# Optimization experiments

Hardware: AMD Instinct MI355X
Metric: run time of the kernel (lower is better)

The kernel has to match this reference:

```python
import jax, jax.numpy as jnp
import numpy as np

B, S, D, H = 2, 2048, 1024, 16
DK = D // H

def setup_inputs() -> dict:
    key = jax.random.key(0)
    ks = jax.random.split(key, 10)
    s = 1.0 / np.sqrt(D)
    x = jax.random.normal(ks[0], (B, S, D), dtype=jnp.float32)
    # causal mask [B,1,S,S]: 1 = keep, 0 = masked
    mask = jnp.broadcast_to(jnp.tril(jnp.ones((S, S), dtype=jnp.int32))[None, None], (B, 1, S, S))
    wq = jax.random.uniform(ks[1], (D, D), jnp.float32, -s, s)
    bq = jax.random.uniform(ks[2], (D,), jnp.float32, -s, s)
    wk = jax.random.uniform(ks[3], (D, D), jnp.float32, -s, s)
    bk = jax.random.uniform(ks[4], (D,), jnp.float32, -s, s)
    wv = jax.random.uniform(ks[5], (D, D), jnp.float32, -s, s)
    bv = jax.random.uniform(ks[6], (D,), jnp.float32, -s, s)
    wo = jax.random.uniform(ks[7], (D, D), jnp.float32, -s, s)
    bo = jax.random.uniform(ks[8], (D,), jnp.float32, -s, s)
    return {"x": x, "mask": mask, "wq": wq, "bq": bq, "wk": wk, "bk": bk,
            "wv": wv, "bv": bv, "wo": wo, "bo": bo}

def reference(x, mask, wq, bq, wk, bk, wv, bv, wo, bo):
    # projections; torch Linear: y = x @ W^T + b
    def proj(w, b):
        return (jnp.einsum('bsd,ed->bse', x, w) + b).reshape(B, S, H, DK).transpose(0, 2, 1, 3)
    q = proj(wq, bq)  # [B,H,S,DK]
    k = proj(wk, bk)
    v = proj(wv, bv)
    scores = jnp.einsum('bhsd,bhtd->bhst', q, k) / np.sqrt(DK)  # [B,H,S,S]
    scores = jnp.where(mask == 0, jnp.float32(-1e9), scores)
    attn = jax.nn.softmax(scores, axis=-1)
    # dropout in eval mode -> identity
    out = jnp.einsum('bhst,bhtd->bhsd', attn, v)  # [B,H,S,DK]
    out = out.transpose(0, 2, 1, 3).reshape(B, S, D)
    return jnp.einsum('bsd,ed->bse', out, wo) + bo
```

## Files before the change

kernel.cpp:

```cpp
#include <hip/hip_runtime.h>
#include <hip/hip_bf16.h>

#define BB 2
#define SS 2048
#define DD 1024
#define HH 16
#define DK 64
#define MM (BB*SS)

typedef __attribute__((ext_vector_type(8))) short bf16x8;
typedef __attribute__((ext_vector_type(4))) float f32x4;

__device__ inline ushort f2bf(float f) {
  __hip_bfloat16 h = __float2bfloat16(f);
  return *reinterpret_cast<ushort*>(&h);
}

__device__ __forceinline__ float exp2_hw(float x) {
  float r; asm("v_exp_f32 %0, %1" : "=v"(r) : "v"(x)); return r;
}

__device__ __forceinline__ void gl_lds16(const ushort* g, ushort* l) {
  __builtin_amdgcn_global_load_lds((const __attribute__((address_space(1))) void*)g,
                                   (__attribute__((address_space(3))) void*)l, 16, 0, 0);
}

__global__ void cvt_f32_bf16(const float* __restrict__ src, ushort* __restrict__ dst, int n4) {
  int i = blockIdx.x * blockDim.x + threadIdx.x;
  int stride = gridDim.x * blockDim.x;
  for (int idx = i; idx < n4; idx += stride) {
    float4 v = reinterpret_cast<const float4*>(src)[idx];
    ushort4 o;
    o.x = f2bf(v.x); o.y = f2bf(v.y); o.z = f2bf(v.z); o.w = f2bf(v.w);
    reinterpret_cast<ushort4*>(dst)[idx] = o;
  }
}

__global__ void cvt3_f32_bf16(const float* __restrict__ s0, const float* __restrict__ s1,
                              const float* __restrict__ s2, ushort* __restrict__ dst) {
  const int n4seg = DD * DD / 4;
  int i = blockIdx.x * blockDim.x + threadIdx.x;
  int stride = gridDim.x * blockDim.x;
  for (int idx = i; idx < 3 * n4seg; idx += stride) {
    int seg = idx / n4seg;
    int off = idx - seg * n4seg;
    const float* s = (seg == 0) ? s0 : (seg == 1) ? s1 : s2;
    float4 v = reinterpret_cast<const float4*>(s)[off];
    ushort4 o;
    o.x = f2bf(v.x); o.y = f2bf(v.y); o.z = f2bf(v.z); o.w = f2bf(v.w);
    reinterpret_cast<ushort4*>(dst)[idx] = o;
  }
}

__global__ void cvt5_f32_bf16(const float* __restrict__ x,
                              const float* __restrict__ s0, const float* __restrict__ s1,
                              const float* __restrict__ s2, const float* __restrict__ s3,
                              ushort* __restrict__ dx, ushort* __restrict__ dw) {
  const int n4x = MM * DD / 4;
  const int n4seg = DD * DD / 4;
  const int total = n4x + 4 * n4seg;
  int i = blockIdx.x * blockDim.x + threadIdx.x;
  int stride = gridDim.x * blockDim.x;
  for (int idx = i; idx < total; idx += stride) {
    float4 v; ushort4* outp;
    if (idx < n4x) {
      v = reinterpret_cast<const float4*>(x)[idx];
      outp = &reinterpret_cast<ushort4*>(dx)[idx];
    } else {
      int widx = idx - n4x;
      int seg = widx / n4seg;
      int off = widx - seg * n4seg;
      const float* s = (seg == 0) ? s0 : (seg == 1) ? s1 : (seg == 2) ? s2 : s3;
      v = reinterpret_cast<const float4*>(s)[off];
      outp = &reinterpret_cast<ushort4*>(dw)[widx];
    }
    ushort4 o;
    o.x = f2bf(v.x); o.y = f2bf(v.y); o.z = f2bf(v.z); o.w = f2bf(v.w);
    *outp = o;
  }
}

__global__ __launch_bounds__(256, 3) void gemm_qkv(const ushort* __restrict__ A,
                                                   const ushort* __restrict__ Wqkv,
                                                   const float* __restrict__ bq,
                                                   const float* __restrict__ bk,
                                                   const float* __restrict__ bv,
                                                   ushort* __restrict__ Qo,
                                                   ushort* __restrict__ Ko,
                                                   ushort* __restrict__ Vo,
                                                   float qscale) {
  constexpr int K = 1024;
  __shared__ __align__(16) ushort lS[2][128 * 64];
  ushort* lA = lS[0];
  ushort* lB = lS[1];
  const int t = threadIdx.x;
  const int w = t >> 6, lane = t & 63;
  const int flat = blockIdx.x + 24 * blockIdx.y;
  const int xcd = flat & 7, idx = flat >> 3;
  const int m0 = ((xcd << 2) + (idx & 3)) * 128;
  const int n0 = (idx >> 2) * 128;
  const int wm = (w >> 1) * 64, wn = (w & 1) * 64;
  const int c = lane & 15, g = lane >> 4;

  f32x4 acc[4][4];
  #pragma unroll
  for (int i = 0; i < 4; i++)
    #pragma unroll
    for (int j = 0; j < 4; j++) acc[i][j] = f32x4{0.f, 0.f, 0.f, 0.f};

  auto stage = [&](int ks) {
    const int k0 = ks * 64;
    #pragma unroll
    for (int i = 0; i < 4; i++) {
      int ch = w * 256 + i * 64 + lane;
      int row = ch >> 3;
      int cs = (ch & 7) ^ (row & 7);
      gl_lds16(&A[(size_t)(m0 + row) * K + k0 + cs * 8], &lA[(w * 256 + i * 64) * 8]);
      gl_lds16(&Wqkv[(size_t)(n0 + row) * K + k0 + cs * 8], &lB[(w * 256 + i * 64) * 8]);
    }
  };

  for (int ks = 0; ks < 16; ks++) {
    stage(ks);
    __syncthreads();
    #pragma unroll
    for (int kk2 = 0; kk2 < 2; kk2++) {
      bf16x8 af[4], bfr[4];
      #pragma unroll
      for (int mi = 0; mi < 4; mi++) {
        int row = wm + mi * 16 + c;
        af[mi] = *reinterpret_cast<const bf16x8*>(&lA[row * 64 + (((kk2 * 4 + g) ^ (c & 7)) * 8)]);
      }
      #pragma unroll
      for (int ni = 0; ni < 4; ni++) {
        int row = wn + ni * 16 + c;
        bfr[ni] = *reinterpret_cast<const bf16x8*>(&lB[row * 64 + (((kk2 * 4 + g) ^ (c & 7)) * 8)]);
      }
      #pragma unroll
      for (int mi = 0; mi < 4; mi++)
        #pragma unroll
        for (int ni = 0; ni < 4; ni++)
          acc[mi][ni] = __builtin_amdgcn_mfma_f32_16x16x32_bf16(af[mi], bfr[ni], acc[mi][ni], 0, 0, 0);
    }
    __syncthreads();
  }

  const int seg = n0 >> 10;
  const float* bp = (seg == 0) ? bq : (seg == 1) ? bk : bv;
  const float sc = (seg == 0) ? qscale : 1.0f;
  ushort* lC = &lS[0][0];

  if (seg < 2) {
    #pragma unroll
    for (int mi = 0; mi < 4; mi++) {
      #pragma unroll
      for (int ni = 0; ni < 4; ni++) {
        int col = wn + ni * 16 + c;
        float bvv = bp[(n0 + col) & 1023];
        #pragma unroll
        for (int j = 0; j < 4; j++) {
          int row = wm + mi * 16 + g * 4 + j;
          lC[row * 128 + col] = f2bf((acc[mi][ni][j] + bvv) * sc);
        }
      }
    }
    __syncthreads();
    ushort* op = (seg == 0) ? Qo : Ko;
    const int b = m0 >> 11, s0r = m0 & 2047;
    #pragma unroll
    for (int i = 0; i < 8; i++) {
      int id = i * 256 + t;
      int row = id >> 4, colblk = id & 15;
      ushort4 v0 = *reinterpret_cast<const ushort4*>(&lC[row * 128 + colblk * 8]);
      ushort4 v1 = *reinterpret_cast<const ushort4*>(&lC[row * 128 + colblk * 8 + 4]);
      int colq = (n0 + colblk * 8) & 1023;
      int h = colq >> 6, dkb = colq & 63;
      ushort* dst = &op[(((size_t)(b * HH + h) * SS + s0r + row) << 6) + dkb];
      reinterpret_cast<ushort4*>(dst)[0] = v0;
      reinterpret_cast<ushort4*>(dst)[1] = v1;
    }
  } else {
    #pragma unroll
    for (int mi = 0; mi < 4; mi++) {
      #pragma unroll
      for (int ni = 0; ni < 4; ni++) {
        int col = wn + ni * 16 + c;
        float bvv = bp[(n0 + col) & 1023];
        int rowbase = wm + mi * 16 + g * 4;
        ushort4 pk;
        pk.x = f2bf(acc[mi][ni][0] + bvv);
        pk.y = f2bf(acc[mi][ni][1] + bvv);
        pk.z = f2bf(acc[mi][ni][2] + bvv);
        pk.w = f2bf(acc[mi][ni][3] + bvv);
        *reinterpret_cast<ushort4*>(&lC[col * 128 + rowbase]) = pk;
      }
    }
    __syncthreads();
    const int b = m0 >> 11, s0r = m0 & 2047;
    #pragma unroll
    for (int i = 0; i < 8; i++) {
      int id = i * 256 + t;
      int col = id >> 4, rowblk = id & 15;
      ushort4 v0 = *reinterpret_cast<const ushort4*>(&lC[col * 128 + rowblk * 8]);
      ushort4 v1 = *reinterpret_cast<const ushort4*>(&lC[col * 128 + rowblk * 8 + 4]);
      int colq = (n0 + col) & 1023;
      int h = colq >> 6, dk = colq & 63;
      ushort* dst = &Vo[(((size_t)(b * HH + h) * DK + dk) << 11) + s0r + rowblk * 8];
      reinterpret_cast<ushort4*>(dst)[0] = v0;
      reinterpret_cast<ushort4*>(dst)[1] = v1;
    }
  }
}

__global__ __launch_bounds__(256, 4) void gemm_out(const ushort* __restrict__ A,
                                                   const ushort* __restrict__ W,
                                                   const float* __restrict__ bias,
                                                   float* __restrict__ out) {
  constexpr int K = 1024;
  __shared__ __align__(16) ushort lA[64 * 64];
  __shared__ __align__(16) ushort lB[64 * 64];
  const int t = threadIdx.x;
  const int w = t >> 6, lane = t & 63;
  const int flat = blockIdx.x + 16 * blockIdx.y;
  const int xcd = flat & 7, idx = flat >> 3;
  const int m0 = ((xcd << 3) + (idx & 7)) * 64;
  const int n0 = (idx >> 3) * 64;
  const int wm = (w >> 1) * 32, wn = (w & 1) * 32;
  const int c = lane & 15, g = lane >> 4;

  f32x4 acc[2][2];
  #pragma unroll
  for (int i = 0; i < 2; i++)
    #pragma unroll
    for (int j = 0; j < 2; j++) acc[i][j] = f32x4{0.f, 0.f, 0.f, 0.f};

  auto stage = [&](int ks) {
    const int k0 = ks * 64;
    #pragma unroll
    for (int i = 0; i < 2; i++) {
      int ch = i * 256 + t;
      int row = ch >> 3;
      int cs = (ch & 7) ^ (row & 7);
      gl_lds16(&A[(size_t)(m0 + row) * K + k0 + cs * 8], &lA[(i * 256 + w * 64) * 8]);
      gl_lds16(&W[(size_t)(n0 + row) * K + k0 + cs * 8], &lB[(i * 256 + w * 64) * 8]);
    }
  };

  for (int ks = 0; ks < 16; ks++) {
    stage(ks);
    __syncthreads();
    #pragma unroll
    for (int kk2 = 0; kk2 < 2; kk2++) {
      bf16x8 af[2], bfr[2];
      #pragma unroll
      for (int mi = 0; mi < 2; mi++) {
        int row = wm + mi * 16 + c;
        af[mi] = *reinterpret_cast<const bf16x8*>(&lA[row * 64 + (((kk2 * 4 + g) ^ (c & 7)) * 8)]);
      }
      #pragma unroll
      for (int ni = 0; ni < 2; ni++) {
        int row = wn + ni * 16 + c;
        bfr[ni] = *reinterpret_cast<const bf16x8*>(&lB[row * 64 + (((kk2 * 4 + g) ^ (c & 7)) * 8)]);
      }
      #pragma unroll
      for (int mi = 0; mi < 2; mi++)
        #pragma unroll
        for (int ni = 0; ni < 2; ni++)
          acc[mi][ni] = __builtin_amdgcn_mfma_f32_16x16x32_bf16(af[mi], bfr[ni], acc[mi][ni], 0, 0, 0);
    }
    __syncthreads();
  }

  #pragma unroll
  for (int mi = 0; mi < 2; mi++) {
    #pragma unroll
    for (int ni = 0; ni < 2; ni++) {
      int colb = n0 + wn + ni * 16 + c;
      float bv = bias[colb];
      #pragma unroll
      for (int j = 0; j < 4; j++) {
        int row = m0 + wm + mi * 16 + g * 4 + j;
        out[(row << 10) + colb] = acc[mi][ni][j] + bv;
      }
    }
  }
}

__global__ __launch_bounds__(256, 2) void attn_fwd(const ushort* __restrict__ Q,
                                                   const ushort* __restrict__ Kk,
                                                   const ushort* __restrict__ Vt,
                                                   ushort* __restrict__ O) {
  __shared__ __align__(16) ushort ldsK[2][2][64 * 64];
  __shared__ __align__(16) ushort ldsV[2][2][64 * 64];
  __shared__ __align__(16) ushort lds_p[4][16 * 72];
  const int t0 = threadIdx.x;
  const int w = t0 >> 6;
  const int lane = t0 & 63;
  const int c = lane & 15, g = lane >> 4;
  const int flat = blockIdx.x + 16 * blockIdx.y;
  const int swz = (flat & 7) * 64 + (flat >> 3);
  const int bx = swz & 15;
  const int bh = swz >> 4;
  const int a = bx * 4 + w;
  const int rb0 = a * 16;
  const int rb1 = 2032 - a * 16;
  const int itB = (2111 - 16 * a) >> 6;
  const int itMax = (2111 - 64 * bx) >> 6;
  const int nS = (itMax + 1) >> 1;

  const ushort* qbase = Q + (size_t)bh * SS * DK;
  const ushort* kbase = Kk + (size_t)bh * SS * DK;
  const ushort* vbase = Vt + (size_t)bh * DK * SS;

  bf16x8 onesf;
  #pragma unroll
  for (int i = 0; i < 8; i++) onesf[i] = (short)0x3F80;

  bf16x8 qf[2][2];
  qf[0][0] = *reinterpret_cast<const bf16x8*>(&qbase[(rb0 + c) * DK + g * 8]);
  qf[0][1] = *reinterpret_cast<const bf16x8*>(&qbase[(rb0 + c) * DK + 32 + g * 8]);
  qf[1][0] = *reinterpret_cast<const bf16x8*>(&qbase[(rb1 + c) * DK + g * 8]);
  qf[1][1] = *reinterpret_cast<const bf16x8*>(&qbase[(rb1 + c) * DK + 32 + g * 8]);

  f32x4 oacc[2][4], lacc[2];
  #pragma unroll
  for (int f = 0; f < 2; f++) {
    #pragma unroll
    for (int i = 0; i < 4; i++) oacc[f][i] = f32x4{0.f, 0.f, 0.f, 0.f};
    lacc[f] = f32x4{0.f, 0.f, 0.f, 0.f};
  }

  auto stage = [&](int st, int buf) {
    #pragma unroll
    for (int half = 0; half < 2; half++) {
      int tt = 2 * st + half; if (tt > 31) tt = 31;
      const int kv = tt * 64;
      #pragma unroll
      for (int i = 0; i < 2; i++) {
        int ch = w * 128 + i * 64 + lane;
        int row = ch >> 3;
        int cs = (ch & 7) ^ (row & 7);
        gl_lds16(&kbase[(kv + row) * DK + cs * 8], &ldsK[buf][half][(w * 128 + i * 64) * 8]);
        gl_lds16(&vbase[row * SS + kv + cs * 8], &ldsV[buf][half][(w * 128 + i * 64) * 8]);
      }
    }
  };

  stage(0, 0);
  __syncthreads();
  int cur = 0;

  for (int st = 0; st < nS; ++st) {
    if (st + 1 < nS) stage(st + 1, cur ^ 1);
    #pragma unroll
    for (int half = 0; half < 2; half++) {
      const int t = 2 * st + half;
      const int kv = t * 64;
      const bool run = t < itMax;
      const bool actB = run && (t < itB);
      const bool actA = run && (kv < rb0 + 16);
      if (actA || actB) {
        bf16x8 kf[8];
        #pragma unroll
        for (int i = 0; i < 8; i++) {
          int tt = i >> 1, kk2 = i & 1;
          kf[i] = *reinterpret_cast<const bf16x8*>(
              &ldsK[cur][half][(tt * 16 + c) * 64 + (((kk2 * 4 + g) ^ (c & 7)) * 8)]);
        }
        f32x4 s[2][4];
        __builtin_amdgcn_s_setprio(1);
        if (actB) {
          #pragma unroll
          for (int tt = 0; tt < 4; tt++) {
            f32x4 z = {0.f, 0.f, 0.f, 0.f};
            z = __builtin_amdgcn_mfma_f32_16x16x32_bf16(qf[1][0], kf[tt * 2], z, 0, 0, 0);
            s[1][tt] = __builtin_amdgcn_mfma_f32_16x16x32_bf16(qf[1][1], kf[tt * 2 + 1], z, 0, 0, 0);
          }
        }
        if (actA) {
          #pragma unroll
          for (int tt = 0; tt < 4; tt++) {
            f32x4 z = {0.f, 0.f, 0.f, 0.f};
            z = __builtin_amdgcn_mfma_f32_16x16x32_bf16(qf[0][0], kf[tt * 2], z, 0, 0, 0);
            s[0][tt] = __builtin_amdgcn_mfma_f32_16x16x32_bf16(qf[0][1], kf[tt * 2 + 1], z, 0, 0, 0);
          }
        }
        __builtin_amdgcn_s_setprio(0);

        bf16x8 vf[8];
        #pragma unroll
        for (int i = 0; i < 8; i++) {
          int dt = i >> 1, kk2 = i & 1;
          vf[i] = *reinterpret_cast<const bf16x8*>(
              &ldsV[cur][half][(dt * 16 + c) * 64 + (((kk2 * 4 + g) ^ (c & 7)) * 8)]);
        }

        ushort* pb = &lds_p[w][0];

        if (actA) {
          const bool edge = (kv + 63 > rb0);
          #pragma unroll
          for (int tt = 0; tt < 4; tt++) {
            int kj = kv + tt * 16 + c;
            #pragma unroll
            for (int j = 0; j < 4; j++) {
              float p = exp2_hw(s[0][tt][j]);
              if (edge && kj > rb0 + g * 4 + j) p = 0.f;
              pb[(g * 4 + j) * 72 + tt * 16 + c] = f2bf(p);
            }
          }
        }
        if (actB) {
          const bool edge = (kv + 63 > rb1);
          #pragma unroll
          for (int tt = 0; tt < 4; tt++) {
            int kj = kv + tt * 16 + c;
            #pragma unroll
            for (int j = 0; j < 4; j++) {
              float p = exp2_hw(s[1][tt][j]);
              if (edge && kj > rb1 + g * 4 + j) p = 0.f;
              s[1][tt][j] = p;
            }
          }
        }
        if (actA) {
          __builtin_amdgcn_s_setprio(1);
          #pragma unroll
          for (int kk2 = 0; kk2 < 2; kk2++) {
            bf16x8 pa = *reinterpret_cast<const bf16x8*>(&pb[c * 72 + kk2 * 32 + g * 8]);
            #pragma unroll
            for (int dt = 0; dt < 4; dt++)
              oacc[0][dt] = __builtin_amdgcn_mfma_f32_16x16x32_bf16(pa, vf[dt * 2 + kk2], oacc[0][dt], 0, 0, 0);
            lacc[0] = __builtin_amdgcn_mfma_f32_16x16x32_bf16(pa, onesf, lacc[0], 0, 0, 0);
          }
          __builtin_amdgcn_s_setprio(0);
        }
        if (actB) {
          #pragma unroll
          for (int tt = 0; tt < 4; tt++) {
            #pragma unroll
            for (int j = 0; j < 4; j++)
              pb[(g * 4 + j) * 72 + tt * 16 + c] = f2bf(s[1][tt][j]);
          }
          __builtin_amdgcn_s_setprio(1);
          #pragma unroll
          for (int kk2 = 0; kk2 < 2; kk2++) {
            bf16x8 pa = *reinterpret_cast<const bf16x8*>(&pb[c * 72 + kk2 * 32 + g * 8]);
            #pragma unroll
            for (int dt = 0; dt < 4; dt++)
              oacc[1][dt] = __builtin_amdgcn_mfma_f32_16x16x32_bf16(pa, vf[dt * 2 + kk2], oacc[1][dt], 0, 0, 0);
            lacc[1] = __builtin_amdgcn_mfma_f32_16x16x32_bf16(pa, onesf, lacc[1], 0, 0, 0);
          }
          __builtin_amdgcn_s_setprio(0);
        }
      }
    }
    __syncthreads();
    cur ^= 1;
  }

  const int b = bh >> 4, h = bh & 15;
  #pragma unroll
  for (int f = 0; f < 2; f++) {
    const int rbf = (f == 0) ? rb0 : rb1;
    #pragma unroll
    for (int j = 0; j < 4; j++) {
      float linv = 1.0f / lacc[f][j];
      int row = rbf + g * 4 + j;
      #pragma unroll
      for (int dt = 0; dt < 4; dt++) {
        float val = oacc[f][dt][j] * linv;
        O[((size_t)(b * SS + row) << 10) + h * DK + dt * 16 + c] = f2bf(val);
      }
    }
  }
}

extern "C" void kernel_launch(void* const* d_in, const int* in_sizes, int n_in,
                              void* d_out, int out_size, void* d_ws, size_t ws_size,
                              hipStream_t stream) {
  const float* x  = (const float*)d_in[0];
  const float* wq = (const float*)d_in[2];
  const float* bq = (const float*)d_in[3];
  const float* wk = (const float*)d_in[4];
  const float* bk = (const float*)d_in[5];
  const float* wv = (const float*)d_in[6];
  const float* bv = (const float*)d_in[7];
  const float* wo = (const float*)d_in[8];
  const float* bo = (const float*)d_in[9];

  ushort* ws = (ushort*)d_ws;
  ushort* xb   = ws;
  ushort* wqkv = xb + (size_t)MM * DD;

  const float qscale = 0.18033688011112043f;
  const size_t needA = (size_t)(4 + 4 + 4 * 4) * DD * DD * sizeof(ushort);

  if (ws_size >= needA) {
    ushort* wob = wqkv + (size_t)3 * DD * DD;
    ushort* qw  = wob + (size_t)DD * DD;
    ushort* kw  = qw + (size_t)MM * DD;
    ushort* vw  = kw + (size_t)MM * DD;
    cvt5_f32_bf16<<<2048, 256, 0, stream>>>(x, wq, wk, wv, wo, xb, wqkv);
    gemm_qkv<<<dim3(24, 32), 256, 0, stream>>>(xb, wqkv, bq, bk, bv, qw, kw, vw, qscale);
    attn_fwd<<<dim3(16, BB * HH), 256, 0, stream>>>(qw, kw, vw, xb);
    gemm_out<<<dim3(16, 64), 256, 0, stream>>>(xb, wob, bo, (float*)d_out);
  } else {
    ushort* qw = wqkv + (size_t)3 * DD * DD;
    ushort* kw = qw + (size_t)MM * DD;
    ushort* vw = kw + (size_t)MM * DD;
    cvt_f32_bf16<<<2048, 256, 0, stream>>>(x, xb, MM * DD / 4);
    cvt3_f32_bf16<<<1536, 256, 0, stream>>>(wq, wk, wv, wqkv);
    gemm_qkv<<<dim3(24, 32), 256, 0, stream>>>(xb, wqkv, bq, bk, bv, qw, kw, vw, qscale);
    cvt_f32_bf16<<<512, 256, 0, stream>>>(wo, wqkv, DD * DD / 4);
    attn_fwd<<<dim3(16, BB * HH), 256, 0, stream>>>(qw, kw, vw, xb);
    gemm_out<<<dim3(16, 64), 256, 0, stream>>>(xb, wqkv, bo, (float*)d_out);
  }
}
```

Baseline: 98.52 us.

## Double-buffer P tiles with XOR-swizzled LDS and batch P writes before PV

The per-wave LDS P buffer is split into two buffers, one per query fragment, and its padded stride is replaced by an XOR swizzle on an unpadded 64-wide row. Both fragments' probabilities are now written to LDS before either PV MFMA block runs. This removes the write-after-read ordering between fragment A's PV and fragment B's P store, letting the scheduler overlap LDS writes with MFMAs. The block-index mapping also flips bx for alternate groups to balance causal workload across concurrently scheduled blocks. The cost is extra LDS per block, which may affect occupancy.

New measurement: 100.0 us. About the same (+1.5%).

```diff
diff --git a/kernel.cpp b/kernel.cpp
--- a/kernel.cpp
+++ b/kernel.cpp
@@ -292,14 +292,14 @@
                                                    ushort* __restrict__ O) {
   __shared__ __align__(16) ushort ldsK[2][2][64 * 64];
   __shared__ __align__(16) ushort ldsV[2][2][64 * 64];
-  __shared__ __align__(16) ushort lds_p[4][16 * 72];
+  __shared__ __align__(16) ushort lds_p[4][2][16 * 64];
   const int t0 = threadIdx.x;
   const int w = t0 >> 6;
   const int lane = t0 & 63;
   const int c = lane & 15, g = lane >> 4;
   const int flat = blockIdx.x + 16 * blockIdx.y;
   const int swz = (flat & 7) * 64 + (flat >> 3);
-  const int bx = swz & 15;
+  const int bx = (swz & 15) ^ (15 * ((swz >> 5) & 1));
   const int bh = swz >> 4;
   const int a = bx * 4 + w;
   const int rb0 = a * 16;
@@ -395,8 +395,6 @@
               &ldsV[cur][half][(dt * 16 + c) * 64 + (((kk2 * 4 + g) ^ (c & 7)) * 8)]);
         }
 
-        ushort* pb = &lds_p[w][0];
-
         if (actA) {
           const bool edge = (kv + 63 > rb0);
           #pragma unroll
@@ -406,7 +404,7 @@
             for (int j = 0; j < 4; j++) {
               float p = exp2_hw(s[0][tt][j]);
               if (edge && kj > rb0 + g * 4 + j) p = 0.f;
-              pb[(g * 4 + j) * 72 + tt * 16 + c] = f2bf(p);
+              s[0][tt][j] = p;
             }
           }
         }
@@ -423,11 +421,34 @@
             }
           }
         }
+        ushort* pb0 = &lds_p[w][0][0];
+        ushort* pb1 = &lds_p[w][1][0];
+        if (actA) {
+          #pragma unroll
+          for (int tt = 0; tt < 4; tt++) {
+            #pragma unroll
+            for (int j = 0; j < 4; j++) {
+              int row = g * 4 + j;
+              pb0[row * 64 + ((tt * 16 + c) ^ ((row & 7) << 3))] = f2bf(s[0][tt][j]);
+            }
+          }
+        }
+        if (actB) {
+          #pragma unroll
+          for (int tt = 0; tt < 4; tt++) {
+            #pragma unroll
+            for (int j = 0; j < 4; j++) {
+              int row = g * 4 + j;
+              pb1[row * 64 + ((tt * 16 + c) ^ ((row & 7) << 3))] = f2bf(s[1][tt][j]);
+            }
+          }
+        }
         if (actA) {
           __builtin_amdgcn_s_setprio(1);
           #pragma unroll
           for (int kk2 = 0; kk2 < 2; kk2++) {
-            bf16x8 pa = *reinterpret_cast<const bf16x8*>(&pb[c * 72 + kk2 * 32 + g * 8]);
+            bf16x8 pa = *reinterpret_cast<const bf16x8*>(
+                &pb0[c * 64 + ((kk2 * 32 + g * 8) ^ ((c & 7) << 3))]);
             #pragma unroll
             for (int dt = 0; dt < 4; dt++)
               oacc[0][dt] = __builtin_amdgcn_mfma_f32_16x16x32_bf16(pa, vf[dt * 2 + kk2], oacc[0][dt], 0, 0, 0);
@@ -436,16 +457,11 @@
           __builtin_amdgcn_s_setprio(0);
         }
         if (actB) {
-          #pragma unroll
-          for (int tt = 0; tt < 4; tt++) {
-            #pragma unroll
-            for (int j = 0; j < 4; j++)
-              pb[(g * 4 + j) * 72 + tt * 16 + c] = f2bf(s[1][tt][j]);
-          }
           __builtin_amdgcn_s_setprio(1);
           #pragma unroll
           for (int kk2 = 0; kk2 < 2; kk2++) {
-            bf16x8 pa = *reinterpret_cast<const bf16x8*>(&pb[c * 72 + kk2 * 32 + g * 8]);
+            bf16x8 pa = *reinterpret_cast<const bf16x8*>(
+                &pb1[c * 64 + ((kk2 * 32 + g * 8) ^ ((c & 7) << 3))]);
             #pragma unroll
             for (int dt = 0; dt < 4; dt++)
               oacc[1][dt] = __builtin_amdgcn_mfma_f32_16x16x32_bf16(pa, vf[dt * 2 + kk2], oacc[1][dt], 0, 0, 0);
```
